# Kernel optimization log

Measured on AMD Instinct MI355X. Metric: run time of the kernel, lower is better.

The kernel has to match this reference:

```python
import jax, jax.numpy as jnp
import numpy as np

J = 24           # joints
CIN_PJ = 4       # channels_in per joint  (C_in = 96)
COUT_PJ = 8      # channels_out per joint (C_out = 192)
K = 15           # kernel size
PAD = 7          # reflect padding on both sides (stride 1 -> T_out == T)
B, T = 128, 4096

NEIGHBOURS = [sorted({max(0, i - 1), i, min(J - 1, i + 1)}) for i in range(J)]

def _build_mask():
    # Block-sparse skeleton neighbour mask over the conv weight.
    mask = np.zeros((J * COUT_PJ, J * CIN_PJ, K), np.float32)
    for i, nb in enumerate(NEIGHBOURS):
        cols = [k * CIN_PJ + c for k in nb for c in range(CIN_PJ)]
        mask[i * COUT_PJ:(i + 1) * COUT_PJ, cols, :] = 1.0
    return jnp.asarray(mask)

MASK = _build_mask()  # [C_out, C_in, K]

def setup_inputs() -> dict:
    key = jax.random.key(0)
    kx, kw, kb = jax.random.split(key, 3)
    x = jax.random.normal(kx, (B, J * CIN_PJ, T), dtype=jnp.float32)
    weight = jax.random.normal(kw, (J * COUT_PJ, J * CIN_PJ, K), dtype=jnp.float32) * 0.05
    bias = jax.random.normal(kb, (J * COUT_PJ,), dtype=jnp.float32) * 0.05
    return {"x": x, "weight": weight, "bias": bias}

def reference(x, weight, bias):
    # weight masked by fixed skeleton-neighbour sparsity every forward pass
    w = weight * MASK
    # reflect-pad the time axis, then VALID conv1d (matches F.pad + conv1d(padding=0))
    xp = jnp.pad(x, ((0, 0), (0, 0), (PAD, PAD)), mode='reflect')
    out = jax.lax.conv_general_dilated(
        xp, w,
        window_strides=(1,),
        padding='VALID',
        dimension_numbers=('NCH', 'OIH', 'NCH'))
    return out + bias[None, :, None]
```

## Files before the change

### kernel.cpp

```cpp
#include <hip/hip_runtime.h>
#include <stdint.h>

#define TLEN  4096
#define BATCH 128
#define NG    6
#define TT    256
#define NIT   4
#define ROWS  272

typedef short short8 __attribute__((ext_vector_type(8)));
typedef float f32x4 __attribute__((ext_vector_type(4)));
typedef unsigned int uint;

__device__ __forceinline__ unsigned short f2bf(float f) {
    uint u = __float_as_uint(f);
    u += 0x7fffu + ((u >> 16) & 1u);
    return (unsigned short)(u >> 16);
}
__device__ __forceinline__ int reflect(int tg) {
    return tg < 0 ? -tg : (tg >= TLEN ? 2 * TLEN - 2 - tg : tg);
}

__global__ __launch_bounds__(256) void prep_weights_kernel(
    const float* __restrict__ w, unsigned short* __restrict__ wf)
{
    int e = blockIdx.x * 256 + threadIdx.x;
    int kk   = e & 255;
    int co_l = (e >> 8) & 15;
    int p    = e >> 12;
    int k    = kk >> 4;
    int ci_l = kk & 15;
    int jo = 2 * p + (co_l >> 3);
    int jn = 2 * p - 1 + (ci_l >> 2);
    int ci_g = 8 * p - 4 + ci_l;
    float v = 0.0f;
    if (k < 15 && jn >= 0 && jn < 24 && jn >= jo - 1 && jn <= jo + 1)
        v = w[((size_t)(16 * p + co_l) * 96 + ci_g) * 15 + k];
    wf[e] = f2bf(v);
}

__global__ __launch_bounds__(256, 3) void skel_conv_kernel(
    const float* __restrict__ x, const unsigned short* __restrict__ wf,
    const float* __restrict__ bias, float* __restrict__ out)
{
    __shared__ __align__(16) unsigned short xlds[2][ROWS * 24];

    const int tid  = threadIdx.x;
    const int tb0  = blockIdx.x * (TT * NIT);
    const int g    = blockIdx.y;
    const int b    = blockIdx.z;
    const int lane = tid & 63;
    const int wave = tid >> 6;
    const int q     = wave & 1;
    const int thalf = wave >> 1;
    const int p     = 2 * g + q;
    const int col  = lane & 15;
    const int hi2  = lane >> 4;

    const int ciBase = 16 * g - 4;
    const float* xb = x + (size_t)b * 96 * TLEN;

    short8 afrag[8];
    {
        const unsigned short* wp = wf + (size_t)(p * 16 + col) * 256 + hi2 * 8;
        #pragma unroll
        for (int s = 0; s < 8; ++s)
            afrag[s] = *reinterpret_cast<const short8*>(wp + s * 32);
    }
    #pragma unroll
    for (int s = 0; s < 8; ++s)
        asm volatile("" : "+v"(afrag[s]));

    const int colb = 4 * hi2;
    float bv[4];
    #pragma unroll
    for (int r = 0; r < 4; ++r) bv[r] = bias[16 * p + colb + r];

    const int hr  = 256 + (tid & 15);
    const int hc0 = tid >> 4;
    const int hc1 = 16 + (tid >> 4);

    float v[24], hv0, hv1;

    auto STAGE_ISSUE = [&](int tt0) {
        int src = reflect(tt0 - 7 + tid);
        const float* xs = xb + src;
        #pragma unroll
        for (int c = 0; c < 24; ++c) {
            int cg = ciBase + c;
            v[c] = ((unsigned)cg < 96u) ? xs[(size_t)cg * TLEN] : 0.f;
        }
        int hsrc = reflect(tt0 - 7 + hr);
        int cg0 = ciBase + hc0;
        hv0 = (hr < 270 && (unsigned)cg0 < 96u) ? xb[(size_t)cg0 * TLEN + hsrc] : 0.f;
        int cg1 = ciBase + hc1;
        hv1 = (tid < 128 && hr < 270 && (unsigned)cg1 < 96u) ? xb[(size_t)cg1 * TLEN + hsrc] : 0.f;
    };

    auto STAGE_WRITE = [&](unsigned short* buf) {
        uint vals[12];
        #pragma unroll
        for (int qq = 0; qq < 12; ++qq)
            vals[qq] = (uint)f2bf(v[2 * qq]) | ((uint)f2bf(v[2 * qq + 1]) << 16);
        *reinterpret_cast<uint4*>(&buf[tid * 24 + 0])  = make_uint4(vals[0], vals[1], vals[2],  vals[3]);
        *reinterpret_cast<uint4*>(&buf[tid * 24 + 8])  = make_uint4(vals[4], vals[5], vals[6],  vals[7]);
        *reinterpret_cast<uint4*>(&buf[tid * 24 + 16]) = make_uint4(vals[8], vals[9], vals[10], vals[11]);
        buf[hr * 24 + hc0] = f2bf(hv0);
        if (tid < 128) buf[hr * 24 + hc1] = f2bf(hv1);
    };

    STAGE_ISSUE(tb0);
    STAGE_WRITE(xlds[0]);
    __syncthreads();

    const int ci0   = 8 * q + 8 * (hi2 & 1);
    const int kb    = hi2 >> 1;
    const int rbase = thalf * 128 + col + kb;

    #pragma unroll
    for (int it = 0; it < NIT; ++it) {
        const unsigned short* buf = xlds[it & 1];

        if (it + 1 < NIT) STAGE_ISSUE(tb0 + (it + 1) * TT);
        __builtin_amdgcn_sched_barrier(0);

        f32x4 acc[8];
        #pragma unroll
        for (int nf = 0; nf < 8; ++nf)
            acc[nf] = (f32x4){bv[0], bv[1], bv[2], bv[3]};

        #pragma unroll
        for (int s = 0; s < 8; ++s) {
            const unsigned short* bp = &buf[(rbase + 2 * s) * 24 + ci0];
            #pragma unroll
            for (int nf = 0; nf < 8; ++nf) {
                short8 bfrag = *reinterpret_cast<const short8*>(bp + nf * (16 * 24));
                acc[nf] = __builtin_amdgcn_mfma_f32_16x16x32_bf16(afrag[s], bfrag, acc[nf], 0, 0, 0);
            }
        }

        if (it + 1 < NIT) STAGE_WRITE(xlds[(it + 1) & 1]);
        __syncthreads();

        float* ob = out + ((size_t)b * 192 + 16 * p + colb) * TLEN
                  + tb0 + it * TT + thalf * 128 + col;
        #pragma unroll
        for (int nf = 0; nf < 8; ++nf) {
            #pragma unroll
            for (int r = 0; r < 4; ++r)
                ob[(size_t)r * TLEN + nf * 16] = acc[nf][r];
        }
    }
}

extern "C" void kernel_launch(void* const* d_in, const int* in_sizes, int n_in,
                              void* d_out, int out_size, void* d_ws, size_t ws_size,
                              hipStream_t stream) {
    const float* x    = (const float*)d_in[0];
    const float* w    = (const float*)d_in[1];
    const float* bias = (const float*)d_in[2];
    float* out        = (float*)d_out;
    unsigned short* wf = (unsigned short*)d_ws;

    prep_weights_kernel<<<dim3(192), dim3(256), 0, stream>>>(w, wf);
    skel_conv_kernel<<<dim3(TLEN / (TT * NIT), NG, BATCH), dim3(256), 0, stream>>>(
        x, wf, bias, out);
}
```

Baseline: 146.0 us.

## Prefetch two stages ahead with dual register buffers and packed bf16 convert

Global loads of the input tile are now issued two iterations ahead into alternating register sets (va/vb), and the LDS write for the next tile happens before the MFMA loop instead of after it. This is meant to give global-load latency a full iteration to resolve and to move LDS stores out of the post-compute critical path. The manual float-to-bf16 rounding is also replaced by the hardware v_cvt_pk_bf16_f32 instruction. The extra 26 live floats per thread raise register pressure, which may hurt occupancy under launch_bounds(256,3). Writing the next buffer right after this iteration's barrier is safe because that buffer was last read in the previous iteration, which ended with a barrier.

```diff
diff --git a/kernel.cpp b/kernel.cpp
--- a/kernel.cpp
+++ b/kernel.cpp
@@ -80,37 +80,45 @@
     const int hc0 = tid >> 4;
     const int hc1 = 16 + (tid >> 4);
 
-    float v[24], hv0, hv1;
+    float va[24], vah0, vah1;
+    float vb[24], vbh0, vbh1;
 
-    auto STAGE_ISSUE = [&](int tt0) {
+    auto STAGE_ISSUE = [&](int tt0, float (&vv)[24], float& h0, float& h1) {
         int src = reflect(tt0 - 7 + tid);
         const float* xs = xb + src;
         #pragma unroll
         for (int c = 0; c < 24; ++c) {
             int cg = ciBase + c;
-            v[c] = ((unsigned)cg < 96u) ? xs[(size_t)cg * TLEN] : 0.f;
+            vv[c] = ((unsigned)cg < 96u) ? xs[(size_t)cg * TLEN] : 0.f;
         }
         int hsrc = reflect(tt0 - 7 + hr);
         int cg0 = ciBase + hc0;
-        hv0 = (hr < 270 && (unsigned)cg0 < 96u) ? xb[(size_t)cg0 * TLEN + hsrc] : 0.f;
+        h0 = (hr < 270 && (unsigned)cg0 < 96u) ? xb[(size_t)cg0 * TLEN + hsrc] : 0.f;
         int cg1 = ciBase + hc1;
-        hv1 = (tid < 128 && hr < 270 && (unsigned)cg1 < 96u) ? xb[(size_t)cg1 * TLEN + hsrc] : 0.f;
+        h1 = (tid < 128 && hr < 270 && (unsigned)cg1 < 96u) ? xb[(size_t)cg1 * TLEN + hsrc] : 0.f;
     };
 
-    auto STAGE_WRITE = [&](unsigned short* buf) {
+    auto STAGE_WRITE = [&](unsigned short* buf, float (&vv)[24], float h0, float h1) {
         uint vals[12];
         #pragma unroll
-        for (int qq = 0; qq < 12; ++qq)
-            vals[qq] = (uint)f2bf(v[2 * qq]) | ((uint)f2bf(v[2 * qq + 1]) << 16);
+        for (int qq = 0; qq < 12; ++qq) {
+            uint r;
+            asm("v_cvt_pk_bf16_f32 %0, %1, %2" : "=v"(r) : "v"(vv[2 * qq]), "v"(vv[2 * qq + 1]));
+            vals[qq] = r;
+        }
         *reinterpret_cast<uint4*>(&buf[tid * 24 + 0])  = make_uint4(vals[0], vals[1], vals[2],  vals[3]);
         *reinterpret_cast<uint4*>(&buf[tid * 24 + 8])  = make_uint4(vals[4], vals[5], vals[6],  vals[7]);
         *reinterpret_cast<uint4*>(&buf[tid * 24 + 16]) = make_uint4(vals[8], vals[9], vals[10], vals[11]);
-        buf[hr * 24 + hc0] = f2bf(hv0);
-        if (tid < 128) buf[hr * 24 + hc1] = f2bf(hv1);
+        uint hp;
+        asm("v_cvt_pk_bf16_f32 %0, %1, %2" : "=v"(hp) : "v"(h0), "v"(h1));
+        buf[hr * 24 + hc0] = (unsigned short)(hp & 0xffffu);
+        if (tid < 128) buf[hr * 24 + hc1] = (unsigned short)(hp >> 16);
     };
 
-    STAGE_ISSUE(tb0);
-    STAGE_WRITE(xlds[0]);
+    STAGE_ISSUE(tb0,      va, vah0, vah1);
+    STAGE_ISSUE(tb0 + TT, vb, vbh0, vbh1);
+    __builtin_amdgcn_sched_barrier(0);
+    STAGE_WRITE(xlds[0], va, vah0, vah1);
     __syncthreads();
 
     const int ci0   = 8 * q + 8 * (hi2 & 1);
@@ -119,10 +127,17 @@
 
     #pragma unroll
     for (int it = 0; it < NIT; ++it) {
+        if ((it & 1) == 0) {
+            if (it + 2 < NIT) STAGE_ISSUE(tb0 + (it + 2) * TT, va, vah0, vah1);
+            __builtin_amdgcn_sched_barrier(0);
+            if (it + 1 < NIT) STAGE_WRITE(xlds[(it + 1) & 1], vb, vbh0, vbh1);
+        } else {
+            if (it + 2 < NIT) STAGE_ISSUE(tb0 + (it + 2) * TT, vb, vbh0, vbh1);
+            __builtin_amdgcn_sched_barrier(0);
+            if (it + 1 < NIT) STAGE_WRITE(xlds[(it + 1) & 1], va, vah0, vah1);
+        }
+
         const unsigned short* buf = xlds[it & 1];
-
-        if (it + 1 < NIT) STAGE_ISSUE(tb0 + (it + 1) * TT);
-        __builtin_amdgcn_sched_barrier(0);
 
         f32x4 acc[8];
         #pragma unroll
@@ -139,7 +154,6 @@
             }
         }
 
-        if (it + 1 < NIT) STAGE_WRITE(xlds[(it + 1) & 1]);
         __syncthreads();
 
         float* ob = out + ((size_t)b * 192 + 16 * p + colb) * TLEN
```

After: 150.0 us. 2.7% more time.

## Double threads per block and redistribute staging loads across 512 threads

Applied to the files above, without the earlier changes.

Raises the block from 256 to 512 threads, so each wave computes 64 time columns instead of 128 and holds half as many accumulators. The global-to-LDS staging is rebalanced so each thread loads two 8-channel units (rows/units from tid/3) instead of a 24-channel row plus halo elements. The aim is more waves in flight, fewer per-thread loads and registers, and better latency hiding. In exchange, block-level barriers now synchronize more waves, and the integer division plus uneven second-unit predicate add some overhead.

```diff
diff --git a/kernel.cpp b/kernel.cpp
--- a/kernel.cpp
+++ b/kernel.cpp
@@ -39,7 +39,7 @@
     wf[e] = f2bf(v);
 }
 
-__global__ __launch_bounds__(256, 3) void skel_conv_kernel(
+__global__ __launch_bounds__(512, 2) void skel_conv_kernel(
     const float* __restrict__ x, const unsigned short* __restrict__ wf,
     const float* __restrict__ bias, float* __restrict__ out)
 {
@@ -51,9 +51,9 @@
     const int b    = blockIdx.z;
     const int lane = tid & 63;
     const int wave = tid >> 6;
-    const int q     = wave & 1;
-    const int thalf = wave >> 1;
-    const int p     = 2 * g + q;
+    const int q    = wave & 1;
+    const int tq   = wave >> 1;
+    const int p    = 2 * g + q;
     const int col  = lane & 15;
     const int hi2  = lane >> 4;
 
@@ -76,37 +76,53 @@
     #pragma unroll
     for (int r = 0; r < 4; ++r) bv[r] = bias[16 * p + colb + r];
 
-    const int hr  = 256 + (tid & 15);
-    const int hc0 = tid >> 4;
-    const int hc1 = 16 + (tid >> 4);
+    const int rowA = tid / 3,         unitA = tid - 3 * rowA;
+    const int slotB = tid + 512;
+    const int rowB = slotB / 3,       unitB = slotB - 3 * rowB;
+    const bool hasB = tid < 304;
 
-    float v[24], hv0, hv1;
+    float vA[8], vB[8];
 
     auto STAGE_ISSUE = [&](int tt0) {
-        int src = reflect(tt0 - 7 + tid);
-        const float* xs = xb + src;
-        #pragma unroll
-        for (int c = 0; c < 24; ++c) {
-            int cg = ciBase + c;
-            v[c] = ((unsigned)cg < 96u) ? xs[(size_t)cg * TLEN] : 0.f;
+        {
+            int src = reflect(tt0 - 7 + rowA);
+            const float* xs = xb + src;
+            int cg0 = ciBase + 8 * unitA;
+            #pragma unroll
+            for (int c = 0; c < 8; ++c) {
+                int cg = cg0 + c;
+                vA[c] = (rowA < 270 && (unsigned)cg < 96u) ? xs[(size_t)cg * TLEN] : 0.f;
+            }
         }
-        int hsrc = reflect(tt0 - 7 + hr);
-        int cg0 = ciBase + hc0;
-        hv0 = (hr < 270 && (unsigned)cg0 < 96u) ? xb[(size_t)cg0 * TLEN + hsrc] : 0.f;
-        int cg1 = ciBase + hc1;
-        hv1 = (tid < 128 && hr < 270 && (unsigned)cg1 < 96u) ? xb[(size_t)cg1 * TLEN + hsrc] : 0.f;
+        if (hasB) {
+            int src = reflect(tt0 - 7 + rowB);
+            const float* xs = xb + src;
+            int cg0 = ciBase + 8 * unitB;
+            #pragma unroll
+            for (int c = 0; c < 8; ++c) {
+                int cg = cg0 + c;
+                vB[c] = (rowB < 270 && (unsigned)cg < 96u) ? xs[(size_t)cg * TLEN] : 0.f;
+            }
+        }
     };
 
     auto STAGE_WRITE = [&](unsigned short* buf) {
-        uint vals[12];
-        #pragma unroll
-        for (int qq = 0; qq < 12; ++qq)
-            vals[qq] = (uint)f2bf(v[2 * qq]) | ((uint)f2bf(v[2 * qq + 1]) << 16);
-        *reinterpret_cast<uint4*>(&buf[tid * 24 + 0])  = make_uint4(vals[0], vals[1], vals[2],  vals[3]);
-        *reinterpret_cast<uint4*>(&buf[tid * 24 + 8])  = make_uint4(vals[4], vals[5], vals[6],  vals[7]);
-        *reinterpret_cast<uint4*>(&buf[tid * 24 + 16]) = make_uint4(vals[8], vals[9], vals[10], vals[11]);
-        buf[hr * 24 + hc0] = f2bf(hv0);
-        if (tid < 128) buf[hr * 24 + hc1] = f2bf(hv1);
+        {
+            uint vals[4];
+            #pragma unroll
+            for (int qq = 0; qq < 4; ++qq)
+                vals[qq] = (uint)f2bf(vA[2 * qq]) | ((uint)f2bf(vA[2 * qq + 1]) << 16);
+            *reinterpret_cast<uint4*>(&buf[rowA * 24 + unitA * 8]) =
+                make_uint4(vals[0], vals[1], vals[2], vals[3]);
+        }
+        if (hasB) {
+            uint vals[4];
+            #pragma unroll
+            for (int qq = 0; qq < 4; ++qq)
+                vals[qq] = (uint)f2bf(vB[2 * qq]) | ((uint)f2bf(vB[2 * qq + 1]) << 16);
+            *reinterpret_cast<uint4*>(&buf[rowB * 24 + unitB * 8]) =
+                make_uint4(vals[0], vals[1], vals[2], vals[3]);
+        }
     };
 
     STAGE_ISSUE(tb0);
@@ -115,7 +131,7 @@
 
     const int ci0   = 8 * q + 8 * (hi2 & 1);
     const int kb    = hi2 >> 1;
-    const int rbase = thalf * 128 + col + kb;
+    const int rbase = tq * 64 + col + kb;
 
     #pragma unroll
     for (int it = 0; it < NIT; ++it) {
@@ -124,16 +140,16 @@
         if (it + 1 < NIT) STAGE_ISSUE(tb0 + (it + 1) * TT);
         __builtin_amdgcn_sched_barrier(0);
 
-        f32x4 acc[8];
+        f32x4 acc[4];
         #pragma unroll
-        for (int nf = 0; nf < 8; ++nf)
+        for (int nf = 0; nf < 4; ++nf)
             acc[nf] = (f32x4){bv[0], bv[1], bv[2], bv[3]};
 
         #pragma unroll
         for (int s = 0; s < 8; ++s) {
             const unsigned short* bp = &buf[(rbase + 2 * s) * 24 + ci0];
             #pragma unroll
-            for (int nf = 0; nf < 8; ++nf) {
+            for (int nf = 0; nf < 4; ++nf) {
                 short8 bfrag = *reinterpret_cast<const short8*>(bp + nf * (16 * 24));
                 acc[nf] = __builtin_amdgcn_mfma_f32_16x16x32_bf16(afrag[s], bfrag, acc[nf], 0, 0, 0);
             }
@@ -143,9 +159,9 @@
         __syncthreads();
 
         float* ob = out + ((size_t)b * 192 + 16 * p + colb) * TLEN
-                  + tb0 + it * TT + thalf * 128 + col;
+                  + tb0 + it * TT + tq * 64 + col;
         #pragma unroll
-        for (int nf = 0; nf < 8; ++nf) {
+        for (int nf = 0; nf < 4; ++nf) {
             #pragma unroll
             for (int r = 0; r < 4; ++r)
                 ob[(size_t)r * TLEN + nf * 16] = acc[nf][r];
@@ -163,6 +179,6 @@
     unsigned short* wf = (unsigned short*)d_ws;
 
     prep_weights_kernel<<<dim3(192), dim3(256), 0, stream>>>(w, wf);
-    skel_conv_kernel<<<dim3(TLEN / (TT * NIT), NG, BATCH), dim3(256), 0, stream>>>(
+    skel_conv_kernel<<<dim3(TLEN / (TT * NIT), NG, BATCH), dim3(512), 0, stream>>>(
         x, wf, bias, out);
 }
```

New measurement: 195.4 us. +33.9%, slower.

## Give each wave a private LDS input window and drop block barriers

Applied to the files above, without the earlier changes.

Instead of the whole block staging a shared double-buffered 24-channel x 272-row tile, each wave now loads and converts only its own 16 input channels over 144 time rows into a private LDS region. Because a wave reads and writes only its own region, and LDS operations within a wave stay in order, the __syncthreads calls are removed and waves can run independently. An interior fast path also skips channel bounds checks. In exchange, overlapping channel and halo data is fetched redundantly across waves, which adds global and L2 traffic. The outer iteration loop is also no longer force-unrolled.

```diff
diff --git a/kernel.cpp b/kernel.cpp
--- a/kernel.cpp
+++ b/kernel.cpp
@@ -6,7 +6,7 @@
 #define NG    6
 #define TT    256
 #define NIT   4
-#define ROWS  272
+#define WROWS 144
 
 typedef short short8 __attribute__((ext_vector_type(8)));
 typedef float f32x4 __attribute__((ext_vector_type(4)));
@@ -43,7 +43,7 @@
     const float* __restrict__ x, const unsigned short* __restrict__ wf,
     const float* __restrict__ bias, float* __restrict__ out)
 {
-    __shared__ __align__(16) unsigned short xlds[2][ROWS * 24];
+    __shared__ __align__(16) unsigned short xlds[4 * WROWS * 24];
 
     const int tid  = threadIdx.x;
     const int tb0  = blockIdx.x * (TT * NIT);
@@ -51,14 +51,16 @@
     const int b    = blockIdx.z;
     const int lane = tid & 63;
     const int wave = tid >> 6;
-    const int q     = wave & 1;
-    const int thalf = wave >> 1;
-    const int p     = 2 * g + q;
+    const int q    = wave & 1;
+    const int h    = wave >> 1;
+    const int p    = 2 * g + q;
     const int col  = lane & 15;
     const int hi2  = lane >> 4;
 
-    const int ciBase = 16 * g - 4;
+    const int ciW = 8 * p - 4;
+    const bool interior = (p >= 1) && (p <= 10);
     const float* xb = x + (size_t)b * 96 * TLEN;
+    unsigned short* mybuf = &xlds[wave * (WROWS * 24)];
 
     short8 afrag[8];
     {
@@ -76,51 +78,61 @@
     #pragma unroll
     for (int r = 0; r < 4; ++r) bv[r] = bias[16 * p + colb + r];
 
-    const int hr  = 256 + (tid & 15);
-    const int hc0 = tid >> 4;
-    const int hc1 = 16 + (tid >> 4);
-
-    float v[24], hv0, hv1;
+    const int rC = 128 + (lane & 15);
+    float vA[16], vB[16], vC[16];
 
     auto STAGE_ISSUE = [&](int tt0) {
-        int src = reflect(tt0 - 7 + tid);
-        const float* xs = xb + src;
-        #pragma unroll
-        for (int c = 0; c < 24; ++c) {
-            int cg = ciBase + c;
-            v[c] = ((unsigned)cg < 96u) ? xs[(size_t)cg * TLEN] : 0.f;
+        int tw = tt0 + h * 128 - 7;
+        const float* xsA = xb + reflect(tw + lane);
+        const float* xsB = xb + reflect(tw + 64 + lane);
+        const float* xsC = xb + reflect(tw + rC);
+        if (interior) {
+            #pragma unroll
+            for (int c = 0; c < 16; ++c) {
+                size_t off = (size_t)(ciW + c) * TLEN;
+                vA[c] = xsA[off];
+                vB[c] = xsB[off];
+                vC[c] = xsC[off];
+            }
+        } else {
+            #pragma unroll
+            for (int c = 0; c < 16; ++c) {
+                int cg = ciW + c;
+                bool ok = (unsigned)cg < 96u;
+                size_t off = (size_t)cg * TLEN;
+                vA[c] = ok ? xsA[off] : 0.f;
+                vB[c] = ok ? xsB[off] : 0.f;
+                vC[c] = ok ? xsC[off] : 0.f;
+            }
         }
-        int hsrc = reflect(tt0 - 7 + hr);
-        int cg0 = ciBase + hc0;
-        hv0 = (hr < 270 && (unsigned)cg0 < 96u) ? xb[(size_t)cg0 * TLEN + hsrc] : 0.f;
-        int cg1 = ciBase + hc1;
-        hv1 = (tid < 128 && hr < 270 && (unsigned)cg1 < 96u) ? xb[(size_t)cg1 * TLEN + hsrc] : 0.f;
     };
 
-    auto STAGE_WRITE = [&](unsigned short* buf) {
-        uint vals[12];
+    auto STAGE_WRITE = [&]() {
+        uint pa[8], pb[8], pc[8];
         #pragma unroll
-        for (int qq = 0; qq < 12; ++qq)
-            vals[qq] = (uint)f2bf(v[2 * qq]) | ((uint)f2bf(v[2 * qq + 1]) << 16);
-        *reinterpret_cast<uint4*>(&buf[tid * 24 + 0])  = make_uint4(vals[0], vals[1], vals[2],  vals[3]);
-        *reinterpret_cast<uint4*>(&buf[tid * 24 + 8])  = make_uint4(vals[4], vals[5], vals[6],  vals[7]);
-        *reinterpret_cast<uint4*>(&buf[tid * 24 + 16]) = make_uint4(vals[8], vals[9], vals[10], vals[11]);
-        buf[hr * 24 + hc0] = f2bf(hv0);
-        if (tid < 128) buf[hr * 24 + hc1] = f2bf(hv1);
+        for (int qq = 0; qq < 8; ++qq) {
+            pa[qq] = (uint)f2bf(vA[2 * qq]) | ((uint)f2bf(vA[2 * qq + 1]) << 16);
+            pb[qq] = (uint)f2bf(vB[2 * qq]) | ((uint)f2bf(vB[2 * qq + 1]) << 16);
+            pc[qq] = (uint)f2bf(vC[2 * qq]) | ((uint)f2bf(vC[2 * qq + 1]) << 16);
+        }
+        *reinterpret_cast<uint4*>(&mybuf[lane * 24 + 0]) = make_uint4(pa[0], pa[1], pa[2], pa[3]);
+        *reinterpret_cast<uint4*>(&mybuf[lane * 24 + 8]) = make_uint4(pa[4], pa[5], pa[6], pa[7]);
+        *reinterpret_cast<uint4*>(&mybuf[(64 + lane) * 24 + 0]) = make_uint4(pb[0], pb[1], pb[2], pb[3]);
+        *reinterpret_cast<uint4*>(&mybuf[(64 + lane) * 24 + 8]) = make_uint4(pb[4], pb[5], pb[6], pb[7]);
+        if (lane < 16) {
+            *reinterpret_cast<uint4*>(&mybuf[rC * 24 + 0]) = make_uint4(pc[0], pc[1], pc[2], pc[3]);
+            *reinterpret_cast<uint4*>(&mybuf[rC * 24 + 8]) = make_uint4(pc[4], pc[5], pc[6], pc[7]);
+        }
     };
 
     STAGE_ISSUE(tb0);
-    STAGE_WRITE(xlds[0]);
-    __syncthreads();
+    STAGE_WRITE();
 
-    const int ci0   = 8 * q + 8 * (hi2 & 1);
+    const int ci0   = 8 * (hi2 & 1);
     const int kb    = hi2 >> 1;
-    const int rbase = thalf * 128 + col + kb;
+    const int rbase = col + kb;
 
-    #pragma unroll
     for (int it = 0; it < NIT; ++it) {
-        const unsigned short* buf = xlds[it & 1];
-
         if (it + 1 < NIT) STAGE_ISSUE(tb0 + (it + 1) * TT);
         __builtin_amdgcn_sched_barrier(0);
 
@@ -131,7 +143,7 @@
 
         #pragma unroll
         for (int s = 0; s < 8; ++s) {
-            const unsigned short* bp = &buf[(rbase + 2 * s) * 24 + ci0];
+            const unsigned short* bp = &mybuf[(rbase + 2 * s) * 24 + ci0];
             #pragma unroll
             for (int nf = 0; nf < 8; ++nf) {
                 short8 bfrag = *reinterpret_cast<const short8*>(bp + nf * (16 * 24));
@@ -139,11 +151,10 @@
             }
         }
 
-        if (it + 1 < NIT) STAGE_WRITE(xlds[(it + 1) & 1]);
-        __syncthreads();
+        if (it + 1 < NIT) STAGE_WRITE();
 
         float* ob = out + ((size_t)b * 192 + 16 * p + colb) * TLEN
-                  + tb0 + it * TT + thalf * 128 + col;
+                  + tb0 + it * TT + h * 128 + col;
         #pragma unroll
         for (int nf = 0; nf < 8; ++nf) {
             #pragma unroll
```

Result: slower. 248.4 us (+70.1%).
